# Kernel tuning notes

Hardware: AMD Instinct MI355X
Metric: run time of the kernel (lower is better)

Reference implementation:

```python
import jax, jax.numpy as jnp
import numpy as np

VOCAB, EMBED, CONV_C, HID, LABELS = 50257, 512, 512, 1024, 128
B, S = 32, 1024

def setup_inputs() -> dict:
    key = jax.random.key(0)
    ks = jax.random.split(key, 8)
    sc = lambda d: 1.0 / np.sqrt(d)
    return {
        "token_ids": jax.random.randint(ks[0], (B, S), 0, VOCAB),
        "emb_table": jax.random.normal(ks[1], (VOCAB, EMBED), jnp.float32) * 0.02,
        "conv_w": jax.random.normal(ks[2], (CONV_C, EMBED), jnp.float32) * sc(EMBED),
        "conv_b": jnp.zeros((CONV_C,), jnp.float32),
        "dec_w1": jax.random.normal(ks[3], (CONV_C, HID), jnp.float32) * sc(CONV_C),
        "dec_b1": jnp.zeros((HID,), jnp.float32),
        "dec_w2": jax.random.normal(ks[4], (HID, LABELS), jnp.float32) * sc(HID),
        "dec_b2": jnp.zeros((LABELS,), jnp.float32),
    }

def reference(token_ids, emb_table, conv_w, conv_b, dec_w1, dec_b1, dec_w2, dec_b2):
    # Embedding lookup: [B, S, E]
    x = emb_table[token_ids]
    # DocNN encoder on a length-1 sequence = kernel-1 conv + relu (+ trivial max-over-time)
    h = jax.nn.relu(jnp.einsum('bse,ce->bsc', x, conv_w) + conv_b)  # [B,S,C]
    # MLP decoder per word
    z = jax.nn.relu(jnp.einsum('bsc,ch->bsh', h, dec_w1) + dec_b1)  # [B,S,H]
    logits = jnp.einsum('bsh,hl->bsl', z, dec_w2) + dec_b2          # [B,S,L]
    # torch.cat over dim 0 of per-word outputs -> flat [B*S, L]
    return logits.reshape(-1, logits.shape[-1])
```

## Files before the change

### kernel.cpp

```cpp
#include <hip/hip_runtime.h>

typedef __bf16 bf16;
typedef __bf16 bf16x4 __attribute__((ext_vector_type(4)));
typedef __bf16 bf16x8 __attribute__((ext_vector_type(8)));
typedef float f32x4 __attribute__((ext_vector_type(4)));

#define NROWS 32768
#define EMBED 512
#define CONV_C 512
#define HID 1024
#define LABELS 128

__device__ inline void async16(const void* g, void* l) {
  __builtin_amdgcn_global_load_lds(
      (const __attribute__((address_space(1))) void*)g,
      (__attribute__((address_space(3))) void*)l, 16, 0, 0);
}

__device__ inline int bitswap02(int g) {
  return ((g & 1) << 2) | (g & 0xA) | ((g >> 2) & 1);
}

__device__ inline bf16x8 cvt8_sw(const float* row, int o0, int o1) {
  f32x4 lo = *(const f32x4*)(row + o0);
  f32x4 hi = *(const f32x4*)(row + o1);
  bf16x8 r;
  r[0] = (bf16)lo[0]; r[1] = (bf16)lo[1]; r[2] = (bf16)lo[2]; r[3] = (bf16)lo[3];
  r[4] = (bf16)hi[0]; r[5] = (bf16)hi[1]; r[6] = (bf16)hi[2]; r[7] = (bf16)hi[3];
  return r;
}


__global__ void cvt_bf16(const float* __restrict__ in, bf16* __restrict__ out, int n) {
  int i = (blockIdx.x * blockDim.x + threadIdx.x) * 4;
  if (i >= n) return;
  float4 v = *(const float4*)(in + i);
  bf16x4 o;
  o.x = (bf16)v.x; o.y = (bf16)v.y; o.z = (bf16)v.z; o.w = (bf16)v.w;
  *(bf16x4*)(out + i) = o;
}

__global__ void transpose_cvt(const float* __restrict__ in, bf16* __restrict__ out,
                              int K, int N) {
  __shared__ float t[64][65];
  int kb = blockIdx.x * 64, nb = blockIdx.y * 64;
  for (int i = threadIdx.x; i < 4096; i += 256) {
    int r = i >> 6, c = i & 63;
    t[r][c] = in[(size_t)(kb + r) * N + nb + c];
  }
  __syncthreads();
  for (int i = threadIdx.x; i < 4096; i += 256) {
    int r = i >> 6, c = i & 63;
    out[(size_t)(nb + r) * K + kb + c] = (bf16)t[c][r];
  }
}

__global__ __launch_bounds__(256) void gemm1_gather(
    const int* __restrict__ tok, const float* __restrict__ emb,
    const bf16* __restrict__ convw, const float* __restrict__ bias,
    bf16* __restrict__ out, int M, int N, int K) {
  __shared__ __attribute__((aligned(16))) char smem[49152];
  const int tid = threadIdx.x;
  const int wave = tid >> 6, lane = tid & 63;
  const int m0 = blockIdx.x * 128, n0 = blockIdx.y * 128;
  const int wm = (wave & 1) * 64, wn = (wave >> 1) * 64;
  const int lrow = lane & 15, quad = lane >> 4;
  const int slot0 = wave * 64 + lane;

  int arow[4], acol[4];
#pragma unroll
  for (int c = 0; c < 4; ++c) {
    int s = slot0 + c * 256;
    int r = s >> 3, p = s & 7;
    arow[c] = r;
    acol[c] = (p ^ (r & 7)) * 4;
  }
  int trow[4];
#pragma unroll
  for (int c = 0; c < 4; ++c) trow[c] = tok[m0 + arow[c]];

  const f32x4 zero4 = {0.f, 0.f, 0.f, 0.f};
  f32x4 acc[4][4];
#pragma unroll
  for (int i = 0; i < 4; ++i)
#pragma unroll
    for (int j = 0; j < 4; ++j) acc[i][j] = zero4;

  auto stage = [&](int p, int k0) {
    float* lAf = (float*)(smem + p * 24576);
    bf16* lB = (bf16*)(smem + p * 24576 + 16384);
#pragma unroll
    for (int c = 0; c < 4; ++c)
      async16(emb + (size_t)trow[c] * EMBED + k0 + acol[c],
              lAf + (size_t)(wave * 64 + c * 256) * 4);
#pragma unroll
    for (int c = 0; c < 2; ++c) {
      int s = slot0 + c * 256;
      int r = s >> 2, cs = s & 3;
      async16(convw + (size_t)(n0 + r) * K + k0 + cs * 8,
              lB + (size_t)(wave * 64 + c * 256) * 8);
    }
  };

  stage(0, 0);
  int cur = 0;
  for (int it = 0; it < 16; ++it) {
    __syncthreads();
    if (it < 15) stage(cur ^ 1, (it + 1) * 32);
    const float* lAf = (const float*)(smem + cur * 24576);
    const bf16* lB = (const bf16*)(smem + cur * 24576 + 16384);

    bf16x8 a[4], b[4];
#pragma unroll
    for (int t = 0; t < 4; ++t) {
      int r = wm + t * 16 + lrow, sw = r & 7;
      a[t] = cvt8_sw(lAf + r * 32, ((2 * quad) ^ sw) * 4, ((2 * quad + 1) ^ sw) * 4);
      b[t] = *(const bf16x8*)(lB + (wn + t * 16 + lrow) * 32 + quad * 8);
    }
#pragma unroll
    for (int mi = 0; mi < 4; ++mi)
#pragma unroll
      for (int ni = 0; ni < 4; ++ni)
        acc[mi][ni] =
            __builtin_amdgcn_mfma_f32_16x16x32_bf16(a[mi], b[ni], acc[mi][ni], 0, 0, 0);
    cur ^= 1;
  }

#pragma unroll
  for (int mi = 0; mi < 4; ++mi) {
#pragma unroll
    for (int ni = 0; ni < 4; ++ni) {
      int col = n0 + wn + ni * 16 + lrow;
      float bv = bias[col];
#pragma unroll
      for (int r = 0; r < 4; ++r) {
        int row = m0 + wm + mi * 16 + quad * 4 + r;
        float v = acc[mi][ni][r] + bv;
        v = v > 0.f ? v : 0.f;
        out[(size_t)row * N + col] = (bf16)v;
      }
    }
  }
}

__global__ __launch_bounds__(512, 2) void gemm23_fused(
    const bf16* __restrict__ h,
    const bf16* __restrict__ w1t,
    const bf16* __restrict__ w2t,
    const float* __restrict__ b1, const float* __restrict__ b2,
    float* __restrict__ out) {
  __shared__ __attribute__((aligned(16))) char smem[131072];
  bf16* zbuf = (bf16*)(smem + 32768);
  const int tid = threadIdx.x, wave = tid >> 6, lane = tid & 63;
  const int m0 = blockIdx.x * 128;
  const int am0 = (wave >> 2) * 64;
  const int bn0 = (wave & 3) * 64;
  const int lb0 = (wave & 3) * 32;
  const int lrow = lane & 15, quad = lane >> 4;
  const int lsw = lrow & 7;
  const int bsw = bitswap02(lsw);

  int a_r[2], a_c[2];
#pragma unroll
  for (int c = 0; c < 2; ++c) {
    int s = tid + c * 512;
    a_r[c] = s >> 3;
    a_c[c] = ((s & 7) ^ (a_r[c] & 7)) * 8;
  }
  int b_r[4], b_c[4];
#pragma unroll
  for (int c = 0; c < 4; ++c) {
    int s = tid + c * 512;
    b_r[c] = s >> 3;
    b_c[c] = ((s & 7) ^ (b_r[c] & 7)) * 8;
  }
  int q_r[2], q_c[2];
#pragma unroll
  for (int c = 0; c < 2; ++c) {
    int s = tid + c * 512;
    q_r[c] = s >> 3;
    q_c[c] = ((s & 7) ^ (q_r[c] & 7)) * 8;
  }

  auto stageA = [&](int p, int k0) {
    bf16* lA = (bf16*)(smem + p * 16384);
#pragma unroll
    for (int c = 0; c < 2; ++c)
      async16(h + (size_t)(m0 + a_r[c]) * 512 + k0 + a_c[c],
              lA + (size_t)(tid + c * 512) * 8);
  };
  auto stageB = [&](int p, int cn0, int k0) {
    bf16* lB = (bf16*)(smem + 32768 + p * 32768);
#pragma unroll
    for (int c = 0; c < 4; ++c)
      async16(w1t + (size_t)(cn0 + b_r[c]) * 512 + k0 + b_c[c],
              lB + (size_t)(tid + c * 512) * 8);
  };
  auto stageQ = [&](int cn0, int qq, int pq) {
    bf16* lQ = (bf16*)(smem + 98304 + pq * 16384);
#pragma unroll
    for (int c = 0; c < 2; ++c)
      async16(w2t + (size_t)q_r[c] * HID + cn0 + qq * 64 + q_c[c],
              lQ + (size_t)(tid + c * 512) * 8);
  };

  const f32x4 zero4 = {0.f, 0.f, 0.f, 0.f};
  f32x4 out_acc[4][2];
#pragma unroll
  for (int i = 0; i < 4; ++i)
#pragma unroll
    for (int j = 0; j < 2; ++j) out_acc[i][j] = zero4;

  auto layer3 = [&](int qq, int pq) {
    const bf16* lQ = (const bf16*)(smem + 98304 + pq * 16384);
#pragma unroll
    for (int ks = 0; ks < 2; ++ks) {
      bf16x8 a3[4], b3[2];
#pragma unroll
      for (int t = 0; t < 4; ++t) {
        int m = am0 + t * 16 + lrow;
        int kq = qq * 8 + ks * 4 + quad;
        a3[t] = *(const bf16x8*)(zbuf + m * 256 + ((kq ^ bsw) << 3));
      }
#pragma unroll
      for (int t = 0; t < 2; ++t) {
        int lab = lb0 + t * 16 + lrow;
        b3[t] = *(const bf16x8*)(lQ + lab * 64 + (((ks * 4 + quad) ^ lsw) * 8));
      }
#pragma unroll
      for (int mi = 0; mi < 4; ++mi)
#pragma unroll
        for (int ni = 0; ni < 2; ++ni)
          out_acc[mi][ni] =
              __builtin_amdgcn_mfma_f32_16x16x32_bf16(a3[mi], b3[ni], out_acc[mi][ni], 0, 0, 0);
    }
  };

  for (int chunk = 0; chunk < 4; ++chunk) {
    const int cn0 = chunk * 256;
    if (chunk == 0) stageA(0, 0);
    stageB(0, cn0, 0);
    stageQ(cn0, 0, 0);

    f32x4 z_acc[4][4];
#pragma unroll
    for (int i = 0; i < 4; ++i)
#pragma unroll
      for (int j = 0; j < 4; ++j) z_acc[i][j] = zero4;

    int cur = 0;
    for (int it = 0; it < 8; ++it) {
      __syncthreads();
      if (it < 7) {
        stageB(cur ^ 1, cn0, (it + 1) * 64);
        stageA(cur ^ 1, (it + 1) * 64);
      }
      const bf16* lA = (const bf16*)(smem + cur * 16384);
      const bf16* lB = (const bf16*)(smem + 32768 + cur * 32768);
#pragma unroll
      for (int ks = 0; ks < 2; ++ks) {
        bf16x8 a[4], b[4];
#pragma unroll
        for (int t = 0; t < 4; ++t)
          a[t] = *(const bf16x8*)(lA + (am0 + t * 16 + lrow) * 64 +
                                  (((ks * 4 + quad) ^ lsw) * 8));
#pragma unroll
        for (int t = 0; t < 4; ++t)
          b[t] = *(const bf16x8*)(lB + (bn0 + t * 16 + lrow) * 64 +
                                  (((ks * 4 + quad) ^ lsw) * 8));
#pragma unroll
        for (int mi = 0; mi < 4; ++mi)
#pragma unroll
          for (int ni = 0; ni < 4; ++ni)
            z_acc[mi][ni] =
                __builtin_amdgcn_mfma_f32_16x16x32_bf16(a[mi], b[ni], z_acc[mi][ni], 0, 0, 0);
      }
      cur ^= 1;
    }

    __syncthreads();
    stageQ(cn0, 1, 1);
#pragma unroll
    for (int mi = 0; mi < 4; ++mi) {
#pragma unroll
      for (int ni = 0; ni < 4; ++ni) {
        int zcol = bn0 + ni * 16 + lrow;
        float bv = b1[cn0 + zcol];
        int q5 = zcol >> 3;
#pragma unroll
        for (int r = 0; r < 4; ++r) {
          int zrow = am0 + mi * 16 + quad * 4 + r;
          float v = z_acc[mi][ni][r] + bv;
          v = v > 0.f ? v : 0.f;
          zbuf[zrow * 256 + ((q5 ^ bitswap02(zrow & 7)) << 3) + (zcol & 7)] = (bf16)v;
        }
      }
    }
    __syncthreads();
    layer3(0, 0);
    __syncthreads();
    stageQ(cn0, 2, 0);
    layer3(1, 1);
    __syncthreads();
    stageQ(cn0, 3, 1);
    if (chunk < 3) stageA(0, 0);
    layer3(2, 0);
    __syncthreads();
    layer3(3, 1);
    __syncthreads();
  }

#pragma unroll
  for (int mi = 0; mi < 4; ++mi) {
#pragma unroll
    for (int ni = 0; ni < 2; ++ni) {
      int col = lb0 + ni * 16 + lrow;
      float bv = b2[col];
#pragma unroll
      for (int r = 0; r < 4; ++r) {
        int row = m0 + am0 + mi * 16 + quad * 4 + r;
        out[(size_t)row * LABELS + col] = out_acc[mi][ni][r] + bv;
      }
    }
  }
}


extern "C" void kernel_launch(void* const* d_in, const int* in_sizes, int n_in,
                              void* d_out, int out_size, void* d_ws, size_t ws_size,
                              hipStream_t stream) {
  const int* tok = (const int*)d_in[0];
  const float* emb = (const float*)d_in[1];
  const float* conv_w = (const float*)d_in[2];
  const float* conv_b = (const float*)d_in[3];
  const float* w1 = (const float*)d_in[4];
  const float* b1 = (const float*)d_in[5];
  const float* w2 = (const float*)d_in[6];
  const float* b2 = (const float*)d_in[7];
  float* out = (float*)d_out;

  char* ws = (char*)d_ws;
  bf16* wtc = (bf16*)(ws);
  bf16* wt1 = (bf16*)(ws + (1u << 19));
  bf16* wt2 = (bf16*)(ws + 3 * (1u << 19));
  bf16* h = (bf16*)(ws + (2u << 20));

  hipLaunchKernelGGL(cvt_bf16, dim3(256), dim3(256), 0, stream,
                     conv_w, wtc, CONV_C * EMBED);
  hipLaunchKernelGGL(transpose_cvt, dim3(8, 16), dim3(256), 0, stream,
                     w1, wt1, CONV_C, HID);
  hipLaunchKernelGGL(transpose_cvt, dim3(16, 2), dim3(256), 0, stream,
                     w2, wt2, HID, LABELS);

  hipLaunchKernelGGL(gemm1_gather, dim3(NROWS / 128, CONV_C / 128), dim3(256),
                     0, stream, tok, emb, wtc, conv_b, h, NROWS, CONV_C, EMBED);
  hipLaunchKernelGGL(gemm23_fused, dim3(NROWS / 128), dim3(512),
                     0, stream, h, wt1, wt2, b1, b2, out);
}
```

Measured before the change: 242.7 us.

## Restructure gather GEMM to cover full output width per row block

The gather+conv GEMM now runs one 512-thread block per 128-row tile. Each block walks the 512 output channels in two 256-wide chunks with a 64-wide K step and XOR-swizzled LDS layouts for both operands. Before, four column blocks each re-gathered the same embedding rows; now each block gathers them twice, which halves the random-row fp32 embedding traffic. The cost is fewer, larger blocks (256 total, about one per CU given 128KB of LDS), which reduces occupancy and the latency hiding available.

```diff
diff --git a/kernel.cpp b/kernel.cpp
--- a/kernel.cpp
+++ b/kernel.cpp
@@ -55,89 +55,112 @@
   }
 }
 
-__global__ __launch_bounds__(256) void gemm1_gather(
+__global__ __launch_bounds__(512, 2) void gemm1_gather(
     const int* __restrict__ tok, const float* __restrict__ emb,
     const bf16* __restrict__ convw, const float* __restrict__ bias,
     bf16* __restrict__ out, int M, int N, int K) {
-  __shared__ __attribute__((aligned(16))) char smem[49152];
-  const int tid = threadIdx.x;
-  const int wave = tid >> 6, lane = tid & 63;
-  const int m0 = blockIdx.x * 128, n0 = blockIdx.y * 128;
-  const int wm = (wave & 1) * 64, wn = (wave >> 1) * 64;
+  __shared__ __attribute__((aligned(16))) char smem[131072];
+  const int tid = threadIdx.x, wave = tid >> 6, lane = tid & 63;
+  const int m0 = blockIdx.x * 128;
+  const int am0 = (wave >> 2) * 64;
+  const int bn0 = (wave & 3) * 64;
   const int lrow = lane & 15, quad = lane >> 4;
-  const int slot0 = wave * 64 + lane;
-
-  int arow[4], acol[4];
+
+  int a_r[4], a_c[4];
 #pragma unroll
   for (int c = 0; c < 4; ++c) {
-    int s = slot0 + c * 256;
-    int r = s >> 3, p = s & 7;
-    arow[c] = r;
-    acol[c] = (p ^ (r & 7)) * 4;
+    int s = tid + c * 512;
+    int r = s >> 4, p = s & 15;
+    a_r[c] = r;
+    a_c[c] = ((((p & 7) ^ (r & 7)) | (p & 8))) * 4;
   }
   int trow[4];
 #pragma unroll
-  for (int c = 0; c < 4; ++c) trow[c] = tok[m0 + arow[c]];
+  for (int c = 0; c < 4; ++c) trow[c] = tok[m0 + a_r[c]];
+
+  int b_r[4], b_c[4];
+#pragma unroll
+  for (int c = 0; c < 4; ++c) {
+    int s = tid + c * 512;
+    b_r[c] = s >> 3;
+    b_c[c] = ((s & 7) ^ (b_r[c] & 7)) * 8;
+  }
+
+  auto stageA = [&](int p, int k0) {
+    float* lAf = (float*)(smem + p * 32768);
+#pragma unroll
+    for (int c = 0; c < 4; ++c)
+      async16(emb + (size_t)trow[c] * EMBED + k0 + a_c[c],
+              lAf + (size_t)(tid + c * 512) * 4);
+  };
+  auto stageB = [&](int p, int cn0, int k0) {
+    bf16* lB = (bf16*)(smem + 65536 + p * 32768);
+#pragma unroll
+    for (int c = 0; c < 4; ++c)
+      async16(convw + (size_t)(cn0 + b_r[c]) * EMBED + k0 + b_c[c],
+              lB + (size_t)(tid + c * 512) * 8);
+  };
 
   const f32x4 zero4 = {0.f, 0.f, 0.f, 0.f};
-  f32x4 acc[4][4];
-#pragma unroll
-  for (int i = 0; i < 4; ++i)
-#pragma unroll
-    for (int j = 0; j < 4; ++j) acc[i][j] = zero4;
-
-  auto stage = [&](int p, int k0) {
-    float* lAf = (float*)(smem + p * 24576);
-    bf16* lB = (bf16*)(smem + p * 24576 + 16384);
-#pragma unroll
-    for (int c = 0; c < 4; ++c)
-      async16(emb + (size_t)trow[c] * EMBED + k0 + acol[c],
-              lAf + (size_t)(wave * 64 + c * 256) * 4);
-#pragma unroll
-    for (int c = 0; c < 2; ++c) {
-      int s = slot0 + c * 256;
-      int r = s >> 2, cs = s & 3;
-      async16(convw + (size_t)(n0 + r) * K + k0 + cs * 8,
-              lB + (size_t)(wave * 64 + c * 256) * 8);
-    }
-  };
-
-  stage(0, 0);
-  int cur = 0;
-  for (int it = 0; it < 16; ++it) {
-    __syncthreads();
-    if (it < 15) stage(cur ^ 1, (it + 1) * 32);
-    const float* lAf = (const float*)(smem + cur * 24576);
-    const bf16* lB = (const bf16*)(smem + cur * 24576 + 16384);
-
-    bf16x8 a[4], b[4];
-#pragma unroll
-    for (int t = 0; t < 4; ++t) {
-      int r = wm + t * 16 + lrow, sw = r & 7;
-      a[t] = cvt8_sw(lAf + r * 32, ((2 * quad) ^ sw) * 4, ((2 * quad + 1) ^ sw) * 4);
-      b[t] = *(const bf16x8*)(lB + (wn + t * 16 + lrow) * 32 + quad * 8);
-    }
-#pragma unroll
-    for (int mi = 0; mi < 4; ++mi)
-#pragma unroll
-      for (int ni = 0; ni < 4; ++ni)
-        acc[mi][ni] =
-            __builtin_amdgcn_mfma_f32_16x16x32_bf16(a[mi], b[ni], acc[mi][ni], 0, 0, 0);
-    cur ^= 1;
-  }
-
-#pragma unroll
-  for (int mi = 0; mi < 4; ++mi) {
-#pragma unroll
-    for (int ni = 0; ni < 4; ++ni) {
-      int col = n0 + wn + ni * 16 + lrow;
-      float bv = bias[col];
-#pragma unroll
-      for (int r = 0; r < 4; ++r) {
-        int row = m0 + wm + mi * 16 + quad * 4 + r;
-        float v = acc[mi][ni][r] + bv;
-        v = v > 0.f ? v : 0.f;
-        out[(size_t)row * N + col] = (bf16)v;
+
+  for (int chunk = 0; chunk < 2; ++chunk) {
+    const int cn0 = chunk * 256;
+    stageA(0, 0);
+    stageB(0, cn0, 0);
+
+    f32x4 acc[4][4];
+#pragma unroll
+    for (int i = 0; i < 4; ++i)
+#pragma unroll
+      for (int j = 0; j < 4; ++j) acc[i][j] = zero4;
+
+    int cur = 0;
+    for (int it = 0; it < 8; ++it) {
+      __syncthreads();
+      if (it < 7) {
+        stageA(cur ^ 1, (it + 1) * 64);
+        stageB(cur ^ 1, cn0, (it + 1) * 64);
+      }
+      const float* lAf = (const float*)(smem + cur * 32768);
+      const bf16* lB = (const bf16*)(smem + 65536 + cur * 32768);
+#pragma unroll
+      for (int ks = 0; ks < 2; ++ks) {
+        bf16x8 a[4], b[4];
+#pragma unroll
+        for (int t = 0; t < 4; ++t) {
+          int r = am0 + t * 16 + lrow, sw = r & 7;
+          int p0 = ks * 8 + ((2 * quad) ^ sw);
+          int p1 = ks * 8 + ((2 * quad + 1) ^ sw);
+          a[t] = cvt8_sw(lAf + r * 64, p0 * 4, p1 * 4);
+        }
+#pragma unroll
+        for (int t = 0; t < 4; ++t) {
+          int rn = bn0 + t * 16 + lrow;
+          b[t] = *(const bf16x8*)(lB + rn * 64 + (((ks * 4 + quad) ^ (rn & 7)) * 8));
+        }
+#pragma unroll
+        for (int mi = 0; mi < 4; ++mi)
+#pragma unroll
+          for (int ni = 0; ni < 4; ++ni)
+            acc[mi][ni] =
+                __builtin_amdgcn_mfma_f32_16x16x32_bf16(a[mi], b[ni], acc[mi][ni], 0, 0, 0);
+      }
+      cur ^= 1;
+    }
+
+#pragma unroll
+    for (int mi = 0; mi < 4; ++mi) {
+#pragma unroll
+      for (int ni = 0; ni < 4; ++ni) {
+        int col = cn0 + bn0 + ni * 16 + lrow;
+        float bv = bias[col];
+#pragma unroll
+        for (int r = 0; r < 4; ++r) {
+          int row = m0 + am0 + mi * 16 + quad * 4 + r;
+          float v = acc[mi][ni][r] + bv;
+          v = v > 0.f ? v : 0.f;
+          out[(size_t)row * CONV_C + col] = (bf16)v;
+        }
       }
     }
   }
@@ -352,7 +375,7 @@
   hipLaunchKernelGGL(transpose_cvt, dim3(16, 2), dim3(256), 0, stream,
                      w2, wt2, HID, LABELS);
 
-  hipLaunchKernelGGL(gemm1_gather, dim3(NROWS / 128, CONV_C / 128), dim3(256),
+  hipLaunchKernelGGL(gemm1_gather, dim3(NROWS / 128), dim3(512),
                      0, stream, tok, emb, wtc, conv_b, h, NROWS, CONV_C, EMBED);
   hipLaunchKernelGGL(gemm23_fused, dim3(NROWS / 128), dim3(512),
                      0, stream, h, wt1, wt2, b1, b2, out);
```

After: 237.1 us. 2.3% less time.

## Fuse gather-conv GEMM into MLP kernel keeping hidden tile in LDS

Applied to the files above, without the earlier changes.

Merges the embedding-gather conv GEMM with the two-layer decoder into one kernel per 128-row tile. The conv output now stays in a 128KB swizzled LDS tile instead of round-tripping through global memory. Weight operands (conv, W1, W2) are now read straight from global/L2 into registers, with no LDS double-buffering. This removes one launch and the h tensor's write and read traffic, but uses 160KB LDS, which limits occupancy. It also risks exposed global-load latency on the weight operands.

```diff
diff --git a/kernel.cpp b/kernel.cpp
--- a/kernel.cpp
+++ b/kernel.cpp
@@ -17,8 +17,11 @@
       (__attribute__((address_space(3))) void*)l, 16, 0, 0);
 }
 
-__device__ inline int bitswap02(int g) {
-  return ((g & 1) << 2) | (g & 0xA) | ((g >> 2) & 1);
+__device__ inline int hpos(int row, int chunk) {
+  return (chunk & 56) | ((chunk & 7) ^ (row & 7));
+}
+__device__ inline int zpos(int row, int chunk) {
+  return (chunk & 8) | ((chunk & 7) ^ (row & 7));
 }
 
 __device__ inline bf16x8 cvt8_sw(const float* row, int o0, int o1) {
@@ -55,192 +58,111 @@
   }
 }
 
-__global__ __launch_bounds__(256) void gemm1_gather(
+__global__ __launch_bounds__(512, 2) void fused_model(
     const int* __restrict__ tok, const float* __restrict__ emb,
-    const bf16* __restrict__ convw, const float* __restrict__ bias,
-    bf16* __restrict__ out, int M, int N, int K) {
-  __shared__ __attribute__((aligned(16))) char smem[49152];
-  const int tid = threadIdx.x;
-  const int wave = tid >> 6, lane = tid & 63;
-  const int m0 = blockIdx.x * 128, n0 = blockIdx.y * 128;
-  const int wm = (wave & 1) * 64, wn = (wave >> 1) * 64;
-  const int lrow = lane & 15, quad = lane >> 4;
-  const int slot0 = wave * 64 + lane;
-
-  int arow[4], acol[4];
-#pragma unroll
-  for (int c = 0; c < 4; ++c) {
-    int s = slot0 + c * 256;
-    int r = s >> 3, p = s & 7;
-    arow[c] = r;
-    acol[c] = (p ^ (r & 7)) * 4;
-  }
-  int trow[4];
-#pragma unroll
-  for (int c = 0; c < 4; ++c) trow[c] = tok[m0 + arow[c]];
-
-  const f32x4 zero4 = {0.f, 0.f, 0.f, 0.f};
-  f32x4 acc[4][4];
-#pragma unroll
-  for (int i = 0; i < 4; ++i)
-#pragma unroll
-    for (int j = 0; j < 4; ++j) acc[i][j] = zero4;
-
-  auto stage = [&](int p, int k0) {
-    float* lAf = (float*)(smem + p * 24576);
-    bf16* lB = (bf16*)(smem + p * 24576 + 16384);
-#pragma unroll
-    for (int c = 0; c < 4; ++c)
-      async16(emb + (size_t)trow[c] * EMBED + k0 + acol[c],
-              lAf + (size_t)(wave * 64 + c * 256) * 4);
-#pragma unroll
-    for (int c = 0; c < 2; ++c) {
-      int s = slot0 + c * 256;
-      int r = s >> 2, cs = s & 3;
-      async16(convw + (size_t)(n0 + r) * K + k0 + cs * 8,
-              lB + (size_t)(wave * 64 + c * 256) * 8);
-    }
-  };
-
-  stage(0, 0);
-  int cur = 0;
-  for (int it = 0; it < 16; ++it) {
-    __syncthreads();
-    if (it < 15) stage(cur ^ 1, (it + 1) * 32);
-    const float* lAf = (const float*)(smem + cur * 24576);
-    const bf16* lB = (const bf16*)(smem + cur * 24576 + 16384);
-
-    bf16x8 a[4], b[4];
-#pragma unroll
-    for (int t = 0; t < 4; ++t) {
-      int r = wm + t * 16 + lrow, sw = r & 7;
-      a[t] = cvt8_sw(lAf + r * 32, ((2 * quad) ^ sw) * 4, ((2 * quad + 1) ^ sw) * 4);
-      b[t] = *(const bf16x8*)(lB + (wn + t * 16 + lrow) * 32 + quad * 8);
-    }
-#pragma unroll
-    for (int mi = 0; mi < 4; ++mi)
-#pragma unroll
-      for (int ni = 0; ni < 4; ++ni)
-        acc[mi][ni] =
-            __builtin_amdgcn_mfma_f32_16x16x32_bf16(a[mi], b[ni], acc[mi][ni], 0, 0, 0);
-    cur ^= 1;
-  }
-
-#pragma unroll
-  for (int mi = 0; mi < 4; ++mi) {
-#pragma unroll
-    for (int ni = 0; ni < 4; ++ni) {
-      int col = n0 + wn + ni * 16 + lrow;
-      float bv = bias[col];
-#pragma unroll
-      for (int r = 0; r < 4; ++r) {
-        int row = m0 + wm + mi * 16 + quad * 4 + r;
-        float v = acc[mi][ni][r] + bv;
-        v = v > 0.f ? v : 0.f;
-        out[(size_t)row * N + col] = (bf16)v;
-      }
-    }
-  }
-}
-
-__global__ __launch_bounds__(512, 2) void gemm23_fused(
-    const bf16* __restrict__ h,
+    const bf16* __restrict__ convw,
+    const float* __restrict__ conv_b,
     const bf16* __restrict__ w1t,
+    const float* __restrict__ b1,
     const bf16* __restrict__ w2t,
-    const float* __restrict__ b1, const float* __restrict__ b2,
+    const float* __restrict__ b2,
     float* __restrict__ out) {
-  __shared__ __attribute__((aligned(16))) char smem[131072];
-  bf16* zbuf = (bf16*)(smem + 32768);
+  __shared__ __attribute__((aligned(16))) char smem[163840];
+  bf16* htile = (bf16*)smem;
+  float* astage = (float*)(smem + 131072);
+  bf16* zbuf = (bf16*)(smem + 131072);
+
   const int tid = threadIdx.x, wave = tid >> 6, lane = tid & 63;
   const int m0 = blockIdx.x * 128;
   const int am0 = (wave >> 2) * 64;
-  const int bn0 = (wave & 3) * 64;
-  const int lb0 = (wave & 3) * 32;
+  const int wn = wave & 3;
+  const int lb0 = wn * 32;
   const int lrow = lane & 15, quad = lane >> 4;
-  const int lsw = lrow & 7;
-  const int bsw = bitswap02(lsw);
 
   int a_r[2], a_c[2];
 #pragma unroll
   for (int c = 0; c < 2; ++c) {
     int s = tid + c * 512;
     a_r[c] = s >> 3;
-    a_c[c] = ((s & 7) ^ (a_r[c] & 7)) * 8;
-  }
-  int b_r[4], b_c[4];
-#pragma unroll
-  for (int c = 0; c < 4; ++c) {
-    int s = tid + c * 512;
-    b_r[c] = s >> 3;
-    b_c[c] = ((s & 7) ^ (b_r[c] & 7)) * 8;
-  }
-  int q_r[2], q_c[2];
-#pragma unroll
-  for (int c = 0; c < 2; ++c) {
-    int s = tid + c * 512;
-    q_r[c] = s >> 3;
-    q_c[c] = ((s & 7) ^ (q_r[c] & 7)) * 8;
-  }
+    a_c[c] = ((s & 7) ^ (a_r[c] & 7)) * 4;
+  }
+  int trow[2];
+#pragma unroll
+  for (int c = 0; c < 2; ++c) trow[c] = tok[m0 + a_r[c]];
 
   auto stageA = [&](int p, int k0) {
-    bf16* lA = (bf16*)(smem + p * 16384);
+    float* lAf = astage + p * 4096;
 #pragma unroll
     for (int c = 0; c < 2; ++c)
-      async16(h + (size_t)(m0 + a_r[c]) * 512 + k0 + a_c[c],
-              lA + (size_t)(tid + c * 512) * 8);
+      async16(emb + (size_t)trow[c] * EMBED + k0 + a_c[c],
+              lAf + (size_t)(tid + c * 512) * 4);
   };
-  auto stageB = [&](int p, int cn0, int k0) {
-    bf16* lB = (bf16*)(smem + 32768 + p * 32768);
-#pragma unroll
-    for (int c = 0; c < 4; ++c)
-      async16(w1t + (size_t)(cn0 + b_r[c]) * 512 + k0 + b_c[c],
-              lB + (size_t)(tid + c * 512) * 8);
-  };
-  auto stageQ = [&](int cn0, int qq, int pq) {
-    bf16* lQ = (bf16*)(smem + 98304 + pq * 16384);
-#pragma unroll
-    for (int c = 0; c < 2; ++c)
-      async16(w2t + (size_t)q_r[c] * HID + cn0 + qq * 64 + q_c[c],
-              lQ + (size_t)(tid + c * 512) * 8);
-  };
 
   const f32x4 zero4 = {0.f, 0.f, 0.f, 0.f};
+
+  for (int nc = 0; nc < 2; ++nc) {
+    const int nc0 = nc * 256;
+    stageA(0, 0);
+
+    f32x4 acc[4][4];
+#pragma unroll
+    for (int i = 0; i < 4; ++i)
+#pragma unroll
+      for (int j = 0; j < 4; ++j) acc[i][j] = zero4;
+
+    int cur = 0;
+    for (int it = 0; it < 16; ++it) {
+      __syncthreads();
+      if (it < 15) stageA(cur ^ 1, (it + 1) * 32);
+      const float* lAf = astage + cur * 4096;
+      bf16x8 a[4], b[4];
+#pragma unroll
+      for (int t = 0; t < 4; ++t) {
+        int r = am0 + t * 16 + lrow;
+        int p0 = (2 * quad) ^ (r & 7);
+        a[t] = cvt8_sw(lAf + r * 32, p0 * 4, (p0 ^ 1) * 4);
+      }
+#pragma unroll
+      for (int t = 0; t < 4; ++t) {
+        int row = nc0 + wn * 64 + t * 16 + lrow;
+        b[t] = *(const bf16x8*)(convw + (size_t)row * EMBED + it * 32 + quad * 8);
+      }
+#pragma unroll
+      for (int mi = 0; mi < 4; ++mi)
+#pragma unroll
+        for (int ni = 0; ni < 4; ++ni)
+          acc[mi][ni] =
+              __builtin_amdgcn_mfma_f32_16x16x32_bf16(a[mi], b[ni], acc[mi][ni], 0, 0, 0);
+      cur ^= 1;
+    }
+
+#pragma unroll
+    for (int mi = 0; mi < 4; ++mi) {
+#pragma unroll
+      for (int ni = 0; ni < 4; ++ni) {
+        int col = nc0 + wn * 64 + ni * 16 + lrow;
+        float bv = conv_b[col];
+        int ch = col >> 3, cw = col & 7;
+#pragma unroll
+        for (int r = 0; r < 4; ++r) {
+          int row = am0 + mi * 16 + quad * 4 + r;
+          float v = acc[mi][ni][r] + bv;
+          v = v > 0.f ? v : 0.f;
+          htile[row * 512 + hpos(row, ch) * 8 + cw] = (bf16)v;
+        }
+      }
+    }
+  }
+  __syncthreads();
+
   f32x4 out_acc[4][2];
 #pragma unroll
   for (int i = 0; i < 4; ++i)
 #pragma unroll
     for (int j = 0; j < 2; ++j) out_acc[i][j] = zero4;
-
-  auto layer3 = [&](int qq, int pq) {
-    const bf16* lQ = (const bf16*)(smem + 98304 + pq * 16384);
-#pragma unroll
-    for (int ks = 0; ks < 2; ++ks) {
-      bf16x8 a3[4], b3[2];
-#pragma unroll
-      for (int t = 0; t < 4; ++t) {
-        int m = am0 + t * 16 + lrow;
-        int kq = qq * 8 + ks * 4 + quad;
-        a3[t] = *(const bf16x8*)(zbuf + m * 256 + ((kq ^ bsw) << 3));
-      }
-#pragma unroll
-      for (int t = 0; t < 2; ++t) {
-        int lab = lb0 + t * 16 + lrow;
-        b3[t] = *(const bf16x8*)(lQ + lab * 64 + (((ks * 4 + quad) ^ lsw) * 8));
-      }
-#pragma unroll
-      for (int mi = 0; mi < 4; ++mi)
-#pragma unroll
-        for (int ni = 0; ni < 2; ++ni)
-          out_acc[mi][ni] =
-              __builtin_amdgcn_mfma_f32_16x16x32_bf16(a3[mi], b3[ni], out_acc[mi][ni], 0, 0, 0);
-    }
-  };
 
   for (int chunk = 0; chunk < 4; ++chunk) {
     const int cn0 = chunk * 256;
-    if (chunk == 0) stageA(0, 0);
-    stageB(0, cn0, 0);
-    stageQ(cn0, 0, 0);
 
     f32x4 z_acc[4][4];
 #pragma unroll
@@ -248,66 +170,73 @@
 #pragma unroll
       for (int j = 0; j < 4; ++j) z_acc[i][j] = zero4;
 
-    int cur = 0;
-    for (int it = 0; it < 8; ++it) {
+#pragma unroll
+    for (int kt = 0; kt < 16; ++kt) {
+      bf16x8 a[4], b[4];
+#pragma unroll
+      for (int t = 0; t < 4; ++t) {
+        int r = am0 + t * 16 + lrow;
+        int c = kt * 4 + quad;
+        a[t] = *(const bf16x8*)(htile + r * 512 + hpos(r, c) * 8);
+      }
+#pragma unroll
+      for (int t = 0; t < 4; ++t) {
+        int row = cn0 + wn * 64 + t * 16 + lrow;
+        b[t] = *(const bf16x8*)(w1t + (size_t)row * 512 + kt * 32 + quad * 8);
+      }
+#pragma unroll
+      for (int mi = 0; mi < 4; ++mi)
+#pragma unroll
+        for (int ni = 0; ni < 4; ++ni)
+          z_acc[mi][ni] =
+              __builtin_amdgcn_mfma_f32_16x16x32_bf16(a[mi], b[ni], z_acc[mi][ni], 0, 0, 0);
+    }
+
+#pragma unroll 1
+    for (int half = 0; half < 2; ++half) {
       __syncthreads();
-      if (it < 7) {
-        stageB(cur ^ 1, cn0, (it + 1) * 64);
-        stageA(cur ^ 1, (it + 1) * 64);
-      }
-      const bf16* lA = (const bf16*)(smem + cur * 16384);
-      const bf16* lB = (const bf16*)(smem + 32768 + cur * 32768);
-#pragma unroll
-      for (int ks = 0; ks < 2; ++ks) {
-        bf16x8 a[4], b[4];
-#pragma unroll
-        for (int t = 0; t < 4; ++t)
-          a[t] = *(const bf16x8*)(lA + (am0 + t * 16 + lrow) * 64 +
-                                  (((ks * 4 + quad) ^ lsw) * 8));
-#pragma unroll
-        for (int t = 0; t < 4; ++t)
-          b[t] = *(const bf16x8*)(lB + (bn0 + t * 16 + lrow) * 64 +
-                                  (((ks * 4 + quad) ^ lsw) * 8));
+      if ((wn >> 1) == half) {
+#pragma unroll
+        for (int mi = 0; mi < 4; ++mi) {
+#pragma unroll
+          for (int ni = 0; ni < 4; ++ni) {
+            int zc = wn * 64 + ni * 16 + lrow - half * 128;
+            float bv = b1[cn0 + wn * 64 + ni * 16 + lrow];
+            int ch = zc >> 3, cw = zc & 7;
+#pragma unroll
+            for (int r = 0; r < 4; ++r) {
+              int zrow = am0 + mi * 16 + quad * 4 + r;
+              float v = z_acc[mi][ni][r] + bv;
+              v = v > 0.f ? v : 0.f;
+              zbuf[zrow * 128 + zpos(zrow, ch) * 8 + cw] = (bf16)v;
+            }
+          }
+        }
+      }
+      __syncthreads();
+#pragma unroll
+      for (int ks = 0; ks < 4; ++ks) {
+        bf16x8 a3[4], b3[2];
+#pragma unroll
+        for (int t = 0; t < 4; ++t) {
+          int r = am0 + t * 16 + lrow;
+          int c = ks * 4 + quad;
+          a3[t] = *(const bf16x8*)(zbuf + r * 128 + zpos(r, c) * 8);
+        }
+#pragma unroll
+        for (int t = 0; t < 2; ++t) {
+          int lab = lb0 + t * 16 + lrow;
+          b3[t] = *(const bf16x8*)(w2t + (size_t)lab * HID + cn0 + half * 128 +
+                                   ks * 32 + quad * 8);
+        }
 #pragma unroll
         for (int mi = 0; mi < 4; ++mi)
 #pragma unroll
-          for (int ni = 0; ni < 4; ++ni)
-            z_acc[mi][ni] =
-                __builtin_amdgcn_mfma_f32_16x16x32_bf16(a[mi], b[ni], z_acc[mi][ni], 0, 0, 0);
-      }
-      cur ^= 1;
-    }
-
-    __syncthreads();
-    stageQ(cn0, 1, 1);
-#pragma unroll
-    for (int mi = 0; mi < 4; ++mi) {
-#pragma unroll
-      for (int ni = 0; ni < 4; ++ni) {
-        int zcol = bn0 + ni * 16 + lrow;
-        float bv = b1[cn0 + zcol];
-        int q5 = zcol >> 3;
-#pragma unroll
-        for (int r = 0; r < 4; ++r) {
-          int zrow = am0 + mi * 16 + quad * 4 + r;
-          float v = z_acc[mi][ni][r] + bv;
-          v = v > 0.f ? v : 0.f;
-          zbuf[zrow * 256 + ((q5 ^ bitswap02(zrow & 7)) << 3) + (zcol & 7)] = (bf16)v;
-        }
-      }
-    }
-    __syncthreads();
-    layer3(0, 0);
-    __syncthreads();
-    stageQ(cn0, 2, 0);
-    layer3(1, 1);
-    __syncthreads();
-    stageQ(cn0, 3, 1);
-    if (chunk < 3) stageA(0, 0);
-    layer3(2, 0);
-    __syncthreads();
-    layer3(3, 1);
-    __syncthreads();
+          for (int ni = 0; ni < 2; ++ni)
+            out_acc[mi][ni] =
+                __builtin_amdgcn_mfma_f32_16x16x32_bf16(a3[mi], b3[ni], out_acc[mi][ni], 0, 0, 0);
+      }
+    }
   }
 
 #pragma unroll
@@ -343,7 +272,6 @@
   bf16* wtc = (bf16*)(ws);
   bf16* wt1 = (bf16*)(ws + (1u << 19));
   bf16* wt2 = (bf16*)(ws + 3 * (1u << 19));
-  bf16* h = (bf16*)(ws + (2u << 20));
 
   hipLaunchKernelGGL(cvt_bf16, dim3(256), dim3(256), 0, stream,
                      conv_w, wtc, CONV_C * EMBED);
@@ -352,8 +280,6 @@
   hipLaunchKernelGGL(transpose_cvt, dim3(16, 2), dim3(256), 0, stream,
                      w2, wt2, HID, LABELS);
 
-  hipLaunchKernelGGL(gemm1_gather, dim3(NROWS / 128, CONV_C / 128), dim3(256),
-                     0, stream, tok, emb, wtc, conv_b, h, NROWS, CONV_C, EMBED);
-  hipLaunchKernelGGL(gemm23_fused, dim3(NROWS / 128), dim3(512),
-                     0, stream, h, wt1, wt2, b1, b2, out);
-}
+  hipLaunchKernelGGL(fused_model, dim3(NROWS / 128), dim3(512),
+                     0, stream, tok, emb, wtc, conv_b, wt1, b1, wt2, b2, out);
+}
```

After: 295.7 us. 1.22x slower.
